# Kernel optimization log

Measured on AMD Instinct MI355X. Metric: run time of the kernel, lower is better.

## Reference

```python
import jax, jax.numpy as jnp
import numpy as np

NUM_EXPERT = 16
D_MODEL = 1024
TOP_K = 2
N_TOKENS = 2048


def setup_inputs() -> dict:
    key = jax.random.key(0)
    k1, k2, k3, k4, k5 = jax.random.split(key, 5)
    inp = jax.random.normal(k1, (N_TOKENS, D_MODEL), dtype=jnp.float32)
    gate_idx = jax.random.randint(k2, (N_TOKENS, TOP_K), 0, NUM_EXPERT, dtype=jnp.int64)
    gate_score = jax.random.uniform(k3, (N_TOKENS, TOP_K), dtype=jnp.float32)
    # per-expert Linear(d_model, d_model) params (fan-in uniform init, like torch)
    bound = 1.0 / np.sqrt(D_MODEL)
    W = jax.random.uniform(k4, (NUM_EXPERT, D_MODEL, D_MODEL), dtype=jnp.float32,
                           minval=-bound, maxval=bound)
    b = jax.random.uniform(k5, (NUM_EXPERT, D_MODEL), dtype=jnp.float32,
                           minval=-bound, maxval=bound)
    return {"inp": inp, "gate_idx": gate_idx, "gate_score": gate_score, "W": W, "b": b}


def reference(inp, gate_idx, gate_score, W, b):
    T, d = inp.shape
    top_k = gate_idx.shape[1]
    # dispatch: repeat each token top_k times -> [T*top_k, d]
    x_rep = jnp.repeat(inp, top_k, axis=0)
    g = gate_idx.reshape(-1)  # [T*top_k]
    # brute-force: every expert applied to every dispatched token, then select
    # outs_all: [E, T*top_k, d]
    outs_all = jnp.einsum('td,edh->eth', x_rep, W) + b[:, None, :]
    expert_out = outs_all[g, jnp.arange(T * top_k)]  # [T*top_k, d]
    # weighted combine: bmm(gate_score[T,1,k], expert_out[T,k,d]) -> [T,d]
    y = jnp.einsum('tk,tkd->td', gate_score, expert_out.reshape(T, top_k, d))
    return y
```

## Files before the change

kernel.cpp:

```cpp
#include <hip/hip_runtime.h>
#include <hip/hip_bf16.h>

#define T_TOKENS 2048
#define DMODEL   1024
#define NEXPERT  16
#define TOPK     2
#define NASSIGN  (T_TOKENS * TOPK)

#define GBM 64
#define GBN 128
#define GBK 64

typedef __attribute__((ext_vector_type(8))) short  short8;
typedef __attribute__((ext_vector_type(4))) float  floatx4;
typedef __attribute__((ext_vector_type(8))) unsigned short ushort8;

__device__ __forceinline__ unsigned short f2bf(float f) {
    unsigned u = __builtin_bit_cast(unsigned, f);
    u += 0x7fff + ((u >> 16) & 1);
    return (unsigned short)(u >> 16);
}

__device__ __forceinline__ void g2l16(const void* g, void* l) {
    __builtin_amdgcn_global_load_lds(
        (__attribute__((address_space(1))) void*)g,
        (__attribute__((address_space(3))) void*)l, 16, 0, 0);
}

__global__ __launch_bounds__(256) void prep(
    const float* __restrict__ x,
    const int*   __restrict__ gate_idx,
    const float* __restrict__ W,
    unsigned short* __restrict__ xbf,
    unsigned short* __restrict__ wbf,
    int* __restrict__ counts, int* __restrict__ offsets, int* __restrict__ list)
{
    __shared__ __align__(16) unsigned short sT[64][72];
    const int bid = blockIdx.x;
    const int t   = threadIdx.x;

    if (bid == 0) {
        int* s_cnt = (int*)&sT[0][0];
        int* s_off = s_cnt + NEXPERT;
        if (t < NEXPERT) s_cnt[t] = 0;
        __syncthreads();
        for (int a = t; a < NASSIGN; a += 256)
            atomicAdd(&s_cnt[gate_idx[a]], 1);
        __syncthreads();
        if (t == 0) {
            int run = 0;
            for (int e = 0; e < NEXPERT; e++) { s_off[e] = run; run += s_cnt[e]; }
        }
        __syncthreads();
        if (t < NEXPERT) {
            counts[t]  = s_cnt[t];
            offsets[t] = s_off[t];
            s_cnt[t]   = s_off[t];
        }
        __syncthreads();
        for (int a = t; a < NASSIGN; a += 256) {
            int e = gate_idx[a];
            list[atomicAdd(&s_cnt[e], 1)] = a;
        }
    } else if (bid <= T_TOKENS / 2) {
        const int tr = (bid - 1) * 2 + (t >> 7);
        const int c  = (t & 127) * 8;
        const float4* p = (const float4*)(x + (size_t)tr * DMODEL + c);
        const float4 v0 = p[0], v1 = p[1];
        __align__(16) unsigned short cv[8];
        cv[0] = f2bf(v0.x); cv[1] = f2bf(v0.y); cv[2] = f2bf(v0.z); cv[3] = f2bf(v0.w);
        cv[4] = f2bf(v1.x); cv[5] = f2bf(v1.y); cv[6] = f2bf(v1.z); cv[7] = f2bf(v1.w);
        *(ushort8*)(xbf + (size_t)tr * DMODEL + c) = *(ushort8*)&cv[0];
    } else {
        const int wb = bid - (T_TOKENS / 2 + 1);
        const int e  = wb >> 8;
        const int k0 = ((wb >> 4) & 15) * 64;
        const int n0 = (wb & 15) * 64;
        const int nl = t & 63;
        const int wv = t >> 6;
        const float* src = W + (size_t)(e * DMODEL + k0 + wv) * DMODEL + n0 + nl;
        #pragma unroll
        for (int i = 0; i < 16; i++)
            sT[nl][i * 4 + wv] = f2bf(src[(size_t)i * 4 * DMODEL]);
        __syncthreads();
        const int nr = t >> 2, kc = t & 3;
        ushort8 v0 = *(const ushort8*)&sT[nr][kc * 16];
        ushort8 v1 = *(const ushort8*)&sT[nr][kc * 16 + 8];
        unsigned short* dst = wbf + (size_t)(e * DMODEL + n0 + nr) * DMODEL + k0 + kc * 16;
        *(ushort8*)dst       = v0;
        *(ushort8*)(dst + 8) = v1;
    }
}

__global__ __launch_bounds__(256) void moe_gemm_bf(
    const unsigned short* __restrict__ xbf,
    const unsigned short* __restrict__ wbf,
    const float* __restrict__ bias,
    const float* __restrict__ score,
    const int*   __restrict__ counts,
    const int*   __restrict__ offsets,
    const int*   __restrict__ list,
    float*       __restrict__ eo)
{
    const int e   = blockIdx.z;
    const int cnt = counts[e];
    const int m0  = blockIdx.y * GBM;
    if (m0 >= cnt) return;
    const int n0  = blockIdx.x * GBN;
    const int off = offsets[e];

    __shared__ __align__(16) unsigned short sA[GBM][GBK];
    __shared__ __align__(16) unsigned short sB[GBN][GBK];

    const int tid  = threadIdx.x;
    const int srow = tid >> 3;
    const int pch  = tid & 7;

    const int ar0 = srow, ar1 = srow + 32;
    const int gm0 = m0 + ar0, gm1 = m0 + ar1;
    const int tok0 = (gm0 < cnt) ? (list[off + gm0] >> 1) : 0;
    const int tok1 = (gm1 < cnt) ? (list[off + gm1] >> 1) : 0;
    const unsigned short* asrc0 = xbf + (size_t)tok0 * DMODEL + (pch ^ (ar0 & 7)) * 8;
    const unsigned short* asrc1 = xbf + (size_t)tok1 * DMODEL + (pch ^ (ar1 & 7)) * 8;

    const unsigned short* wbbase = wbf + (size_t)e * DMODEL * DMODEL;
    const unsigned short* bsrc[4];
    #pragma unroll
    for (int i = 0; i < 4; i++) {
        const int row = i * 32 + srow;
        bsrc[i] = wbbase + (size_t)(n0 + row) * DMODEL + (pch ^ (row & 7)) * 8;
    }

    char* lA = (char*)&sA[0][0] + tid * 16;
    char* lB = (char*)&sB[0][0] + tid * 16;

    const int wave = tid >> 6;
    const int lane = tid & 63;
    const int wn   = wave * 32;
    const int fr   = lane & 15;
    const int quad = lane >> 4;

    floatx4 acc[4][2] = {};

    for (int k0 = 0; k0 < DMODEL; k0 += GBK) {
        g2l16(asrc0 + k0, lA);
        g2l16(asrc1 + k0, lA + 4096);
        g2l16(bsrc[0] + k0, lB);
        g2l16(bsrc[1] + k0, lB + 4096);
        g2l16(bsrc[2] + k0, lB + 8192);
        g2l16(bsrc[3] + k0, lB + 12288);
        __syncthreads();

        #pragma unroll
        for (int kk = 0; kk < 2; kk++) {
            const int cc = (kk * 4 + quad) ^ (fr & 7);
            short8 af[4], bf[2];
            #pragma unroll
            for (int mi = 0; mi < 4; mi++)
                af[mi] = *(const short8*)&sA[mi * 16 + fr][cc * 8];
            #pragma unroll
            for (int ni = 0; ni < 2; ni++)
                bf[ni] = *(const short8*)&sB[wn + ni * 16 + fr][cc * 8];
            #pragma unroll
            for (int mi = 0; mi < 4; mi++)
                #pragma unroll
                for (int ni = 0; ni < 2; ni++)
                    acc[mi][ni] = __builtin_amdgcn_mfma_f32_16x16x32_bf16(
                        af[mi], bf[ni], acc[mi][ni], 0, 0, 0);
        }
        __syncthreads();
    }

    const int colA = n0 + wn + fr;
    const int colB = colA + 16;
    const float bv0 = bias[e * DMODEL + colA];
    const float bv1 = bias[e * DMODEL + colB];
    #pragma unroll
    for (int mi = 0; mi < 4; mi++) {
        const int rb = mi * 16 + quad * 4;
        #pragma unroll
        for (int r = 0; r < 4; r++) {
            const int gm = m0 + rb + r;
            if (gm >= cnt) continue;
            const int a = list[off + gm];
            const float s = score[a];
            float* row = eo + (size_t)a * DMODEL;
            row[colA] = s * (acc[mi][0][r] + bv0);
            row[colB] = s * (acc[mi][1][r] + bv1);
        }
    }
}

__global__ __launch_bounds__(256) void combine(const float* __restrict__ eo,
                                               float* __restrict__ out) {
    const int t = blockIdx.x;
    const int d = threadIdx.x * 4;
    const float4 a = *(const float4*)(eo + (size_t)(2 * t)     * DMODEL + d);
    const float4 b = *(const float4*)(eo + (size_t)(2 * t + 1) * DMODEL + d);
    *(float4*)(out + (size_t)t * DMODEL + d) =
        make_float4(a.x + b.x, a.y + b.y, a.z + b.z, a.w + b.w);
}

#define LDSK 72
__global__ __launch_bounds__(256) void moe_gemm_inline(
    const float* __restrict__ x, const float* __restrict__ W,
    const float* __restrict__ bias, const float* __restrict__ score,
    const int* __restrict__ counts, const int* __restrict__ offsets,
    const int* __restrict__ list, float* __restrict__ dst)
{
    const int e   = blockIdx.z;
    const int cnt = counts[e];
    const int m0  = blockIdx.y * 64;
    if (m0 >= cnt) return;
    const int n0  = blockIdx.x * 64;
    const int off = offsets[e];

    __shared__ __align__(16) unsigned short sA[64][LDSK];
    __shared__ __align__(16) unsigned short sB[64][LDSK];

    const int tid = threadIdx.x;
    const int arow = tid >> 2, aq = tid & 3, acol = aq * 16;
    const bool avalid = (m0 + arow) < cnt;
    int atok = 0;
    if (avalid) atok = list[off + m0 + arow] >> 1;
    const float* xsrc = x + (size_t)atok * DMODEL + acol;

    const int bk = tid >> 2, bng = tid & 3, bn = bng * 16, rot = tid & 15;
    const float* wsrc = W + (size_t)(e * DMODEL + bk) * DMODEL + n0 + bn;

    const int wave = tid >> 6, lane = tid & 63;
    const int wn = wave * 16, fr = lane & 15, quad = lane >> 4;

    floatx4 acc[4] = {};

    for (int k0 = 0; k0 < DMODEL; k0 += 64) {
        {
            float4 v[4];
            if (avalid) {
                const float4* p = (const float4*)(xsrc + k0);
                v[0] = p[0]; v[1] = p[1]; v[2] = p[2]; v[3] = p[3];
            } else {
                v[0] = v[1] = v[2] = v[3] = make_float4(0.f, 0.f, 0.f, 0.f);
            }
            __align__(16) unsigned short cvt[16];
            #pragma unroll
            for (int i = 0; i < 4; i++) {
                cvt[4*i+0] = f2bf(v[i].x); cvt[4*i+1] = f2bf(v[i].y);
                cvt[4*i+2] = f2bf(v[i].z); cvt[4*i+3] = f2bf(v[i].w);
            }
            *(ushort8*)&sA[arow][acol]     = *(ushort8*)&cvt[0];
            *(ushort8*)&sA[arow][acol + 8] = *(ushort8*)&cvt[8];
        }
        {
            const float4* p = (const float4*)(wsrc + (size_t)k0 * DMODEL);
            float4 v[4];
            v[0] = p[0]; v[1] = p[1]; v[2] = p[2]; v[3] = p[3];
            unsigned short cvt[16];
            #pragma unroll
            for (int i = 0; i < 4; i++) {
                cvt[4*i+0] = f2bf(v[i].x); cvt[4*i+1] = f2bf(v[i].y);
                cvt[4*i+2] = f2bf(v[i].z); cvt[4*i+3] = f2bf(v[i].w);
            }
            #pragma unroll
            for (int i = 0; i < 16; i++) {
                int m = (i + rot) & 15;
                sB[bn + m][bk] = cvt[m];
            }
        }
        __syncthreads();
        #pragma unroll
        for (int kk = 0; kk < 2; kk++) {
            const int ko = kk * 32 + quad * 8;
            short8 af[4], bf;
            #pragma unroll
            for (int mi = 0; mi < 4; mi++)
                af[mi] = *(const short8*)&sA[mi * 16 + fr][ko];
            bf = *(const short8*)&sB[wn + fr][ko];
            #pragma unroll
            for (int mi = 0; mi < 4; mi++)
                acc[mi] = __builtin_amdgcn_mfma_f32_16x16x32_bf16(af[mi], bf, acc[mi], 0, 0, 0);
        }
        __syncthreads();
    }

    const int col = n0 + wn + fr;
    const float bv = bias[e * DMODEL + col];
    #pragma unroll
    for (int mi = 0; mi < 4; mi++) {
        const int rb = mi * 16 + quad * 4;
        #pragma unroll
        for (int r = 0; r < 4; r++) {
            const int gm = m0 + rb + r;
            if (gm >= cnt) continue;
            const int a = list[off + gm];
            atomicAdd(&dst[(size_t)(a >> 1) * DMODEL + col],
                      score[a] * (acc[mi][r] + bv));
        }
    }
}

extern "C" void kernel_launch(void* const* d_in, const int* in_sizes, int n_in,
                              void* d_out, int out_size, void* d_ws, size_t ws_size,
                              hipStream_t stream) {
    const float* x    = (const float*)d_in[0];
    const int*   gidx = (const int*)d_in[1];
    const float* gsc  = (const float*)d_in[2];
    const float* W    = (const float*)d_in[3];
    const float* bias = (const float*)d_in[4];
    float* out = (float*)d_out;

    int* ws      = (int*)d_ws;
    int* counts  = ws;
    int* offsets = ws + 16;
    int* list    = ws + 32;

    const size_t eo_off  = 32 * 1024;
    const size_t eo_sz   = (size_t)NASSIGN * DMODEL * sizeof(float);
    const size_t xbf_off = eo_off + eo_sz;
    const size_t xbf_sz  = (size_t)T_TOKENS * DMODEL * sizeof(unsigned short);
    const size_t wbf_off = xbf_off + xbf_sz;
    const size_t wbf_sz  = (size_t)NEXPERT * DMODEL * DMODEL * sizeof(unsigned short);
    const size_t need_full = wbf_off + wbf_sz;

    float*          eo  = (float*)((char*)d_ws + eo_off);
    unsigned short* xbf = (unsigned short*)((char*)d_ws + xbf_off);
    unsigned short* wbf = (unsigned short*)((char*)d_ws + wbf_off);

    if (ws_size >= need_full) {
        prep<<<1 + T_TOKENS / 2 + NEXPERT * 16 * 16, 256, 0, stream>>>(
            x, gidx, W, xbf, wbf, counts, offsets, list);
        dim3 grid(DMODEL / GBN, 512 / GBM, NEXPERT);
        moe_gemm_bf<<<grid, 256, 0, stream>>>(xbf, wbf, bias, gsc,
                                              counts, offsets, list, eo);
        combine<<<T_TOKENS, 256, 0, stream>>>(eo, out);
    } else {
        prep<<<1, 256, 0, stream>>>(x, gidx, W, (unsigned short*)0, (unsigned short*)0,
                                    counts, offsets, list);
        hipMemsetAsync(d_out, 0, (size_t)T_TOKENS * DMODEL * sizeof(float), stream);
        dim3 grid(DMODEL / 64, 512 / 64, NEXPERT);
        moe_gemm_inline<<<grid, 256, 0, stream>>>(x, W, bias, gsc,
                                                  counts, offsets, list, out);
    }
}
```

Measured before the change: 146.6 us.

## Split MoE GEMM over K into two partial buffers and rotate transpose writes

The expert GEMM grid is doubled by splitting the K dimension in two. Each half writes its partial result to a separate expert-output buffer, with the bias added only in the first half, and the combine kernel sums four partial rows per token. This is meant to raise the block count for better CU occupancy on the small per-expert GEMMs, at the cost of twice the fp32 intermediate writes and reads. Separately, the weight-transpose loop in prep rotates its store order per lane, apparently to reduce LDS bank conflicts.

```diff
diff --git a/kernel.cpp b/kernel.cpp
--- a/kernel.cpp
+++ b/kernel.cpp
@@ -10,6 +10,8 @@
 #define GBM 64
 #define GBN 128
 #define GBK 64
+#define KSPLIT 2
+#define KCH (DMODEL / KSPLIT)
 
 typedef __attribute__((ext_vector_type(8))) short  short8;
 typedef __attribute__((ext_vector_type(4))) float  floatx4;
@@ -79,9 +81,12 @@
         const int nl = t & 63;
         const int wv = t >> 6;
         const float* src = W + (size_t)(e * DMODEL + k0 + wv) * DMODEL + n0 + nl;
-        #pragma unroll
-        for (int i = 0; i < 16; i++)
-            sT[nl][i * 4 + wv] = f2bf(src[(size_t)i * 4 * DMODEL]);
+        const int rot = (nl + (nl >> 4)) & 15;
+        #pragma unroll
+        for (int i = 0; i < 16; i++) {
+            const int j = (i + rot) & 15;
+            sT[nl][j * 4 + wv] = f2bf(src[(size_t)j * 4 * DMODEL]);
+        }
         __syncthreads();
         const int nr = t >> 2, kc = t & 3;
         ushort8 v0 = *(const ushort8*)&sT[nr][kc * 16];
@@ -102,7 +107,8 @@
     const int*   __restrict__ list,
     float*       __restrict__ eo)
 {
-    const int e   = blockIdx.z;
+    const int e   = blockIdx.z >> 1;
+    const int kc  = blockIdx.z & 1;
     const int cnt = counts[e];
     const int m0  = blockIdx.y * GBM;
     if (m0 >= cnt) return;
@@ -142,7 +148,9 @@
 
     floatx4 acc[4][2] = {};
 
-    for (int k0 = 0; k0 < DMODEL; k0 += GBK) {
+    const int kbeg = kc * KCH;
+    const int kend = kbeg + KCH;
+    for (int k0 = kbeg; k0 < kend; k0 += GBK) {
         g2l16(asrc0 + k0, lA);
         g2l16(asrc1 + k0, lA + 4096);
         g2l16(bsrc[0] + k0, lB);
@@ -173,8 +181,10 @@
 
     const int colA = n0 + wn + fr;
     const int colB = colA + 16;
-    const float bv0 = bias[e * DMODEL + colA];
-    const float bv1 = bias[e * DMODEL + colB];
+    const float bflag = (kc == 0) ? 1.0f : 0.0f;
+    const float bv0 = bflag * bias[e * DMODEL + colA];
+    const float bv1 = bflag * bias[e * DMODEL + colB];
+    float* eobase = eo + (size_t)kc * NASSIGN * DMODEL;
     #pragma unroll
     for (int mi = 0; mi < 4; mi++) {
         const int rb = mi * 16 + quad * 4;
@@ -184,7 +194,7 @@
             if (gm >= cnt) continue;
             const int a = list[off + gm];
             const float s = score[a];
-            float* row = eo + (size_t)a * DMODEL;
+            float* row = eobase + (size_t)a * DMODEL;
             row[colA] = s * (acc[mi][0][r] + bv0);
             row[colB] = s * (acc[mi][1][r] + bv1);
         }
@@ -195,10 +205,16 @@
                                                float* __restrict__ out) {
     const int t = blockIdx.x;
     const int d = threadIdx.x * 4;
-    const float4 a = *(const float4*)(eo + (size_t)(2 * t)     * DMODEL + d);
-    const float4 b = *(const float4*)(eo + (size_t)(2 * t + 1) * DMODEL + d);
+    const size_t half = (size_t)NASSIGN * DMODEL;
+    const float4 a0 = *(const float4*)(eo + (size_t)(2 * t)     * DMODEL + d);
+    const float4 a1 = *(const float4*)(eo + (size_t)(2 * t + 1) * DMODEL + d);
+    const float4 b0 = *(const float4*)(eo + half + (size_t)(2 * t)     * DMODEL + d);
+    const float4 b1 = *(const float4*)(eo + half + (size_t)(2 * t + 1) * DMODEL + d);
     *(float4*)(out + (size_t)t * DMODEL + d) =
-        make_float4(a.x + b.x, a.y + b.y, a.z + b.z, a.w + b.w);
+        make_float4(a0.x + a1.x + b0.x + b1.x,
+                    a0.y + a1.y + b0.y + b1.y,
+                    a0.z + a1.z + b0.z + b1.z,
+                    a0.w + a1.w + b0.w + b1.w);
 }
 
 #define LDSK 72
@@ -315,7 +331,7 @@
     int* list    = ws + 32;
 
     const size_t eo_off  = 32 * 1024;
-    const size_t eo_sz   = (size_t)NASSIGN * DMODEL * sizeof(float);
+    const size_t eo_sz   = (size_t)KSPLIT * NASSIGN * DMODEL * sizeof(float);
     const size_t xbf_off = eo_off + eo_sz;
     const size_t xbf_sz  = (size_t)T_TOKENS * DMODEL * sizeof(unsigned short);
     const size_t wbf_off = xbf_off + xbf_sz;
@@ -329,7 +345,7 @@
     if (ws_size >= need_full) {
         prep<<<1 + T_TOKENS / 2 + NEXPERT * 16 * 16, 256, 0, stream>>>(
             x, gidx, W, xbf, wbf, counts, offsets, list);
-        dim3 grid(DMODEL / GBN, 512 / GBM, NEXPERT);
+        dim3 grid(DMODEL / GBN, 512 / GBM, NEXPERT * KSPLIT);
         moe_gemm_bf<<<grid, 256, 0, stream>>>(xbf, wbf, bias, gsc,
                                               counts, offsets, list, eo);
         combine<<<T_TOKENS, 256, 0, stream>>>(eo, out);
```

Result: slower. 155.9 us (+6.3%).

## Store expert outputs in bf16 and vectorize weight conversion loads

Applied to the files above, without the earlier changes.

The intermediate expert-output buffer is now stored as bf16 instead of fp32, which halves the scatter writes from the GEMM and the reads in the combine kernel. The weight conversion in prep now reads float4 vectors along N rather than scalar strided loads, to make global reads coalesced and wide. The fallback path gets a dedicated routing kernel. Rounding the intermediates to bf16 adds some precision loss before the final sum.

```diff
diff --git a/kernel.cpp b/kernel.cpp
--- a/kernel.cpp
+++ b/kernel.cpp
@@ -14,11 +14,15 @@
 typedef __attribute__((ext_vector_type(8))) short  short8;
 typedef __attribute__((ext_vector_type(4))) float  floatx4;
 typedef __attribute__((ext_vector_type(8))) unsigned short ushort8;
+typedef __attribute__((ext_vector_type(4))) unsigned short usv4;
 
 __device__ __forceinline__ unsigned short f2bf(float f) {
     unsigned u = __builtin_bit_cast(unsigned, f);
     u += 0x7fff + ((u >> 16) & 1);
     return (unsigned short)(u >> 16);
+}
+__device__ __forceinline__ float bf2f(unsigned short s) {
+    return __builtin_bit_cast(float, (unsigned)s << 16);
 }
 
 __device__ __forceinline__ void g2l16(const void* g, void* l) {
@@ -76,12 +80,18 @@
         const int e  = wb >> 8;
         const int k0 = ((wb >> 4) & 15) * 64;
         const int n0 = (wb & 15) * 64;
-        const int nl = t & 63;
-        const int wv = t >> 6;
-        const float* src = W + (size_t)(e * DMODEL + k0 + wv) * DMODEL + n0 + nl;
-        #pragma unroll
-        for (int i = 0; i < 16; i++)
-            sT[nl][i * 4 + wv] = f2bf(src[(size_t)i * 4 * DMODEL]);
+        const int ks = t >> 4;
+        const int nq = (t & 15) * 4;
+        const float* srcbase = W + ((size_t)(e * DMODEL + k0 + ks)) * DMODEL + n0 + nq;
+        #pragma unroll
+        for (int c = 0; c < 4; c++) {
+            const int k = c * 16 + ks;
+            const float4 v = *(const float4*)(srcbase + (size_t)c * 16 * DMODEL);
+            sT[nq + 0][k] = f2bf(v.x);
+            sT[nq + 1][k] = f2bf(v.y);
+            sT[nq + 2][k] = f2bf(v.z);
+            sT[nq + 3][k] = f2bf(v.w);
+        }
         __syncthreads();
         const int nr = t >> 2, kc = t & 3;
         ushort8 v0 = *(const ushort8*)&sT[nr][kc * 16];
@@ -100,7 +110,7 @@
     const int*   __restrict__ counts,
     const int*   __restrict__ offsets,
     const int*   __restrict__ list,
-    float*       __restrict__ eo)
+    unsigned short* __restrict__ eo)
 {
     const int e   = blockIdx.z;
     const int cnt = counts[e];
@@ -184,21 +194,52 @@
             if (gm >= cnt) continue;
             const int a = list[off + gm];
             const float s = score[a];
-            float* row = eo + (size_t)a * DMODEL;
-            row[colA] = s * (acc[mi][0][r] + bv0);
-            row[colB] = s * (acc[mi][1][r] + bv1);
-        }
-    }
-}
-
-__global__ __launch_bounds__(256) void combine(const float* __restrict__ eo,
+            unsigned short* row = eo + (size_t)a * DMODEL;
+            row[colA] = f2bf(s * (acc[mi][0][r] + bv0));
+            row[colB] = f2bf(s * (acc[mi][1][r] + bv1));
+        }
+    }
+}
+
+__global__ __launch_bounds__(256) void combine(const unsigned short* __restrict__ eo,
                                                float* __restrict__ out) {
     const int t = blockIdx.x;
     const int d = threadIdx.x * 4;
-    const float4 a = *(const float4*)(eo + (size_t)(2 * t)     * DMODEL + d);
-    const float4 b = *(const float4*)(eo + (size_t)(2 * t + 1) * DMODEL + d);
+    const usv4 a = *(const usv4*)(eo + (size_t)(2 * t)     * DMODEL + d);
+    const usv4 b = *(const usv4*)(eo + (size_t)(2 * t + 1) * DMODEL + d);
     *(float4*)(out + (size_t)t * DMODEL + d) =
-        make_float4(a.x + b.x, a.y + b.y, a.z + b.z, a.w + b.w);
+        make_float4(bf2f(a.x) + bf2f(b.x), bf2f(a.y) + bf2f(b.y),
+                    bf2f(a.z) + bf2f(b.z), bf2f(a.w) + bf2f(b.w));
+}
+
+__global__ void build_routing(const int* __restrict__ gate_idx,
+                              int* __restrict__ counts,
+                              int* __restrict__ offsets,
+                              int* __restrict__ list) {
+    __shared__ int s_cnt[NEXPERT];
+    __shared__ int s_off[NEXPERT];
+    const int tid = threadIdx.x;
+    if (tid < NEXPERT) s_cnt[tid] = 0;
+    __syncthreads();
+    for (int a = tid; a < NASSIGN; a += blockDim.x)
+        atomicAdd(&s_cnt[gate_idx[a]], 1);
+    __syncthreads();
+    if (tid == 0) {
+        int run = 0;
+        for (int e = 0; e < NEXPERT; e++) { s_off[e] = run; run += s_cnt[e]; }
+    }
+    __syncthreads();
+    if (tid < NEXPERT) {
+        counts[tid]  = s_cnt[tid];
+        offsets[tid] = s_off[tid];
+        s_cnt[tid]   = s_off[tid];
+    }
+    __syncthreads();
+    for (int a = tid; a < NASSIGN; a += blockDim.x) {
+        int e = gate_idx[a];
+        int pos = atomicAdd(&s_cnt[e], 1);
+        list[pos] = a;
+    }
 }
 
 #define LDSK 72
@@ -315,14 +356,14 @@
     int* list    = ws + 32;
 
     const size_t eo_off  = 32 * 1024;
-    const size_t eo_sz   = (size_t)NASSIGN * DMODEL * sizeof(float);
+    const size_t eo_sz   = (size_t)NASSIGN * DMODEL * sizeof(unsigned short);
     const size_t xbf_off = eo_off + eo_sz;
     const size_t xbf_sz  = (size_t)T_TOKENS * DMODEL * sizeof(unsigned short);
     const size_t wbf_off = xbf_off + xbf_sz;
     const size_t wbf_sz  = (size_t)NEXPERT * DMODEL * DMODEL * sizeof(unsigned short);
     const size_t need_full = wbf_off + wbf_sz;
 
-    float*          eo  = (float*)((char*)d_ws + eo_off);
+    unsigned short* eo  = (unsigned short*)((char*)d_ws + eo_off);
     unsigned short* xbf = (unsigned short*)((char*)d_ws + xbf_off);
     unsigned short* wbf = (unsigned short*)((char*)d_ws + wbf_off);
 
@@ -334,8 +375,7 @@
                                               counts, offsets, list, eo);
         combine<<<T_TOKENS, 256, 0, stream>>>(eo, out);
     } else {
-        prep<<<1, 256, 0, stream>>>(x, gidx, W, (unsigned short*)0, (unsigned short*)0,
-                                    counts, offsets, list);
+        build_routing<<<1, 256, 0, stream>>>(gidx, counts, offsets, list);
         hipMemsetAsync(d_out, 0, (size_t)T_TOKENS * DMODEL * sizeof(float), stream);
         dim3 grid(DMODEL / 64, 512 / 64, NEXPERT);
         moe_gemm_inline<<<grid, 256, 0, stream>>>(x, W, bias, gsc,
```

Measured after the change: 145.4 us. About the same (-0.9%).
